# Kernel tuning notes

Measured on AMD Instinct MI355X. Metric: run time of the kernel, lower is better.

The kernel has to match this reference:

```python
import jax, jax.numpy as jnp
import numpy as np
import math

B, S, C = 4, 2048, 128
H, DK, DV, K = 8, 64, 64, 3


def setup_inputs() -> dict:
    key = jax.random.key(0)
    ks = jax.random.split(key, 12)
    sd = 0.05
    return {
        "x": jax.random.normal(ks[0], (B, S, C), dtype=jnp.float32),
        "length": jax.random.randint(ks[1], (B,), 1, S + 1, dtype=jnp.int32),
        "wq": jax.random.normal(ks[2], (H * DK, C, K), dtype=jnp.float32) * sd,
        "bq": jnp.zeros((H * DK,), dtype=jnp.float32),
        "wk": jax.random.normal(ks[3], (H * DK, C, K), dtype=jnp.float32) * sd,
        "bk": jnp.zeros((H * DK,), dtype=jnp.float32),
        "wv": jax.random.normal(ks[4], (H * DV, C), dtype=jnp.float32) * sd,
        "bv": jnp.zeros((H * DV,), dtype=jnp.float32),
        "w1": jax.random.normal(ks[5], (DV, H * DV), dtype=jnp.float32) * sd,
        "b1": jnp.zeros((DV,), dtype=jnp.float32),
        "w2": jax.random.normal(ks[6], (1, DV), dtype=jnp.float32) * sd,
        "b2": jnp.zeros((1,), dtype=jnp.float32),
    }


def _causal_conv(x, w, b):
    # x: (b,s,c), w: (o,c,k) torch Conv1d layout -> (b,s,o), causal (left) padding
    y = jax.lax.conv_general_dilated(
        x.transpose(0, 2, 1), w, window_strides=(1,), padding=[(K - 1, 0)],
        dimension_numbers=("NCH", "OIH", "NCH"))
    return y.transpose(0, 2, 1) + b


def _split_heads(x, d):
    b, s, _ = x.shape
    return x.reshape(b, s, H, d).transpose(0, 2, 1, 3)  # (b,h,s,d)


def reference(x, length, wq, bq, wk, bk, wv, bv, w1, b1, w2, b2):
    q = _split_heads(_causal_conv(x, wq, bq), DK)            # (b,h,s,dk)
    k = _split_heads(_causal_conv(x, wk, bk), DK)            # (b,h,s,dk)
    v = _split_heads(jax.nn.relu(x @ wv.T + bv), DV)         # (b,h,s,dv)

    attn = jnp.einsum("bhqd,bhkd->bhqk", q, k) / math.sqrt(DK)
    # future mask: additive -1e9 above the diagonal (matches triu * -1e9 + softmax)
    future = jnp.triu(jnp.ones((S, S), dtype=attn.dtype), k=1) * (-1e9)
    score = jax.nn.softmax(attn + future, axis=-1)
    # padding mask: zero query rows >= length[b]
    row_valid = (jnp.arange(S)[None, :] < length[:, None]).astype(score.dtype)
    score = score * row_valid[:, None, :, None]              # (b,h,s,s)

    out1 = jnp.einsum("bhqk,bhkd->bhqd", score, v)           # (b,h,s,dv)
    out2 = out1.transpose(0, 2, 1, 3).reshape(x.shape[0], S, H * DV)
    out3 = jax.nn.relu(out2 @ w1.T + b1) @ w2.T + b2         # (b,s,1)
    return out3, score
```

## Files before the change

### kernel.cpp

```cpp
#include <hip/hip_runtime.h>

#define S_ 2048
#define C_ 128
#define B_ 4
#define H_ 8
#define D_ 64

typedef __attribute__((ext_vector_type(8))) short bf16x8;
typedef __attribute__((ext_vector_type(4))) float f32x4;

__device__ inline unsigned short f2bf(float f) {
    union { float f; unsigned int u; } c; c.f = f;
    unsigned int u = c.u;
    unsigned int r = (u + 0x7FFFu + ((u >> 16) & 1u)) >> 16;
    return (unsigned short)r;
}
__device__ inline float bf2f(unsigned short s) {
    union { unsigned int u; float f; } c; c.u = ((unsigned int)s) << 16;
    return c.f;
}

__global__ __launch_bounds__(256) void prep_kernel(
    const float* __restrict__ x,
    const float* __restrict__ wq, const float* __restrict__ wk,
    const float* __restrict__ wv, const float* __restrict__ w1,
    unsigned short* __restrict__ xh,
    unsigned short* __restrict__ wPackQ, unsigned short* __restrict__ wPackK,
    unsigned short* __restrict__ wPackV, float* __restrict__ w1T)
{
    int idx = blockIdx.x * 256 + threadIdx.x;
    if (idx < 1048576) {
        xh[idx] = f2bf(x[idx]);
    } else if (idx < 1245184) {
        int i = idx - 1048576;
        int t = i >> 16, r = i & 65535;
        int o = r >> 7, c = r & 127;
        wPackQ[i] = f2bf(wq[o * 384 + c * 3 + t]);
    } else if (idx < 1441792) {
        int i = idx - 1245184;
        int t = i >> 16, r = i & 65535;
        int o = r >> 7, c = r & 127;
        wPackK[i] = f2bf(wk[o * 384 + c * 3 + t]);
    } else if (idx < 1507328) {
        int i = idx - 1441792;
        wPackV[i] = f2bf(wv[i]);
    } else if (idx < 1540096) {
        int i = idx - 1507328;
        int j = i >> 6, d = i & 63;
        w1T[i] = w1[d * 512 + j];
    }
}

__global__ __launch_bounds__(256) void qkv_kernel(
    const unsigned short* __restrict__ xh,
    const unsigned short* __restrict__ wPackQ, const unsigned short* __restrict__ wPackK,
    const unsigned short* __restrict__ wPackV,
    const float* __restrict__ bq, const float* __restrict__ bk,
    const float* __restrict__ bv,
    unsigned short* __restrict__ Qh, unsigned short* __restrict__ Kh,
    unsigned short* __restrict__ VhT)
{
    __shared__ __align__(16) short xs[130 * 136];
    __shared__ __align__(16) short ws[64 * 136];

    int s0 = blockIdx.x * 128;
    int h = blockIdx.y;
    int b = blockIdx.z;
    int bh = b * H_ + h;
    int tid = threadIdx.x;
    int w = tid >> 6;
    int lane = tid & 63;
    int col = lane & 15;
    int quad = lane >> 4;

    for (int i = tid; i < 2080; i += 256) {
        int row = i >> 4, c8 = (i & 15) << 3;
        int s = s0 - 2 + row;
        uint4 v = {0u, 0u, 0u, 0u};
        if (s >= 0) v = *(const uint4*)&xh[((long)b * S_ + s) * C_ + c8];
        *(uint4*)&xs[row * 136 + c8] = v;
    }

    for (int sec = 0; sec < 3; sec++) {
        const unsigned short* wsel = (sec == 0) ? wPackQ : (sec == 1) ? wPackK : wPackV;
        int tlo = (sec == 2) ? 2 : 0;

        f32x4 acc[2][4];
        #pragma unroll
        for (int rt = 0; rt < 2; rt++)
            #pragma unroll
            for (int nt = 0; nt < 4; nt++) acc[rt][nt] = (f32x4){0.f, 0.f, 0.f, 0.f};

        for (int t = tlo; t < 3; t++) {
            if (!(sec == 0 && t == 0)) __syncthreads();
            long wbase = (sec == 2) ? ((long)h * 8192)
                                    : ((long)t * 65536 + (long)h * 8192);
            for (int i = tid; i < 1024; i += 256) {
                int row = i >> 4, c8 = (i & 15) << 3;
                *(uint4*)&ws[row * 136 + c8] = *(const uint4*)&wsel[wbase + row * 128 + c8];
            }
            __syncthreads();

            #pragma unroll
            for (int kc = 0; kc < 4; kc++) {
                int ko = kc * 32 + quad * 8;
                bf16x8 a0 = *(const bf16x8*)&xs[(w * 32 + col + t) * 136 + ko];
                bf16x8 a1 = *(const bf16x8*)&xs[(w * 32 + 16 + col + t) * 136 + ko];
                #pragma unroll
                for (int nt = 0; nt < 4; nt++) {
                    bf16x8 bfr = *(const bf16x8*)&ws[(nt * 16 + col) * 136 + ko];
                    acc[0][nt] = __builtin_amdgcn_mfma_f32_16x16x32_bf16(a0, bfr, acc[0][nt], 0, 0, 0);
                    acc[1][nt] = __builtin_amdgcn_mfma_f32_16x16x32_bf16(a1, bfr, acc[1][nt], 0, 0, 0);
                }
            }
        }

        if (sec == 0) {
            #pragma unroll
            for (int nt = 0; nt < 4; nt++) {
                float bias = bq[h * 64 + nt * 16 + col];
                #pragma unroll
                for (int rt = 0; rt < 2; rt++)
                    #pragma unroll
                    for (int r = 0; r < 4; r++) {
                        int s = s0 + w * 32 + rt * 16 + quad * 4 + r;
                        Qh[((long)bh * S_ + s) * D_ + nt * 16 + col] =
                            f2bf((acc[rt][nt][r] + bias) * 0.125f);
                    }
            }
        } else if (sec == 1) {
            #pragma unroll
            for (int nt = 0; nt < 4; nt++) {
                float bias = bk[h * 64 + nt * 16 + col];
                #pragma unroll
                for (int rt = 0; rt < 2; rt++)
                    #pragma unroll
                    for (int r = 0; r < 4; r++) {
                        int s = s0 + w * 32 + rt * 16 + quad * 4 + r;
                        Kh[((long)bh * S_ + s) * D_ + nt * 16 + col] =
                            f2bf(acc[rt][nt][r] + bias);
                    }
            }
        } else {
            __syncthreads();
            #pragma unroll
            for (int nt = 0; nt < 4; nt++) {
                float bias = bv[h * 64 + nt * 16 + col];
                #pragma unroll
                for (int rt = 0; rt < 2; rt++)
                    #pragma unroll
                    for (int r = 0; r < 4; r++) {
                        int sl = w * 32 + rt * 16 + quad * 4 + r;
                        ws[(nt * 16 + col) * 136 + sl] =
                            (short)f2bf(fmaxf(acc[rt][nt][r] + bias, 0.f));
                    }
            }
            __syncthreads();
            for (int i = tid; i < 1024; i += 256) {
                int row = i >> 4, c8 = (i & 15) << 3;
                *(uint4*)&VhT[((long)bh * D_ + row) * S_ + s0 + c8] =
                    *(const uint4*)&ws[row * 136 + c8];
            }
        }
    }
}

#define PST 78
__global__ __launch_bounds__(256) void attn_kernel(
    const unsigned short* __restrict__ Qh, const unsigned short* __restrict__ Kh,
    const unsigned short* __restrict__ VhT, const int* __restrict__ length,
    float* __restrict__ score, float* __restrict__ out2)
{
    __shared__ __align__(16) short Kbuf[2][64 * 72];
    __shared__ __align__(16) short Pfh[64 * PST];

    int idx = blockIdx.x;
    int xcd = idx & 7;
    int slot = idx >> 3;
    int t = slot >> 2;
    int qt = (t < 16) ? t : 47 - t;
    int bh = xcd * 4 + (slot & 3);
    int b = bh >> 3, h = bh & 7;
    int q0 = qt * 64;
    int tid = threadIdx.x;
    int w = tid >> 6;
    int lane = tid & 63;
    int col = lane & 15;
    int quad = lane >> 4;
    int len = length[b];

    const unsigned short* Qb = Qh + (long)bh * S_ * D_;
    const unsigned short* Kb = Kh + (long)bh * S_ * D_;
    const unsigned short* Vtb = VhT + (long)bh * D_ * S_;
    float* scb = score + (long)bh * S_ * S_;

    int srow_ = tid >> 2, sc16_ = (tid & 3) * 16;

    {
        *(uint4*)&Pfh[srow_ * PST + sc16_]     = *(const uint4*)&Qb[(q0 + srow_) * D_ + sc16_];
        *(uint4*)&Pfh[srow_ * PST + sc16_ + 8] = *(const uint4*)&Qb[(q0 + srow_) * D_ + sc16_ + 8];
    }
    __syncthreads();
    int arow = w * 16 + col;
    bf16x8 aq0 = *(const bf16x8*)&Pfh[arow * PST + quad * 8];
    bf16x8 aq1 = *(const bf16x8*)&Pfh[arow * PST + 32 + quad * 8];

    float lrun[4];
    #pragma unroll
    for (int r = 0; r < 4; r++) lrun[r] = 0.f;

    {
        *(uint4*)&Kbuf[0][srow_ * 72 + sc16_]     = *(const uint4*)&Kb[srow_ * D_ + sc16_];
        *(uint4*)&Kbuf[0][srow_ * 72 + sc16_ + 8] = *(const uint4*)&Kb[srow_ * D_ + sc16_ + 8];
    }
    __syncthreads();

    for (int kt = 0; kt <= qt; kt++) {
        int buf = kt & 1;
        if (kt < qt) {
            *(uint4*)&Kbuf[1 - buf][srow_ * 72 + sc16_] =
                *(const uint4*)&Kb[((kt + 1) * 64 + srow_) * D_ + sc16_];
            *(uint4*)&Kbuf[1 - buf][srow_ * 72 + sc16_ + 8] =
                *(const uint4*)&Kb[((kt + 1) * 64 + srow_) * D_ + sc16_ + 8];
        }

        f32x4 acc[4];
        #pragma unroll
        for (int n = 0; n < 4; n++) acc[n] = (f32x4){0.f, 0.f, 0.f, 0.f};
        #pragma unroll
        for (int n = 0; n < 4; n++) {
            bf16x8 b0 = *(const bf16x8*)&Kbuf[buf][(n * 16 + col) * 72 + quad * 8];
            acc[n] = __builtin_amdgcn_mfma_f32_16x16x32_bf16(aq0, b0, acc[n], 0, 0, 0);
            bf16x8 b1 = *(const bf16x8*)&Kbuf[buf][(n * 16 + col) * 72 + 32 + quad * 8];
            acc[n] = __builtin_amdgcn_mfma_f32_16x16x32_bf16(aq1, b1, acc[n], 0, 0, 0);
        }
        if (kt == qt) {
            #pragma unroll
            for (int n = 0; n < 4; n++) {
                int kk = kt * 64 + n * 16 + col;
                #pragma unroll
                for (int r = 0; r < 4; r++) {
                    int q = q0 + w * 16 + quad * 4 + r;
                    if (kk > q) acc[n][r] = -1.0e30f;
                }
            }
        }
        #pragma unroll
        for (int r = 0; r < 4; r++) {
            lrun[r] += __expf(acc[0][r]) + __expf(acc[1][r]) +
                       __expf(acc[2][r]) + __expf(acc[3][r]);
        }
        __syncthreads();
    }

    #pragma unroll
    for (int off = 1; off < 16; off <<= 1) {
        #pragma unroll
        for (int r = 0; r < 4; r++) lrun[r] += __shfl_xor(lrun[r], off, 64);
    }
    float linv[4];
    #pragma unroll
    for (int r = 0; r < 4; r++) linv[r] = 1.0f / lrun[r];

    f32x4 oacc[4];
    #pragma unroll
    for (int n = 0; n < 4; n++) oacc[n] = (f32x4){0.f, 0.f, 0.f, 0.f};

    for (int kt = 0; kt <= qt; kt++) {
        __syncthreads();
        {
            *(uint4*)&Kbuf[0][srow_ * 72 + sc16_] =
                *(const uint4*)&Kb[(kt * 64 + srow_) * D_ + sc16_];
            *(uint4*)&Kbuf[0][srow_ * 72 + sc16_ + 8] =
                *(const uint4*)&Kb[(kt * 64 + srow_) * D_ + sc16_ + 8];
            *(uint4*)&Kbuf[1][srow_ * 72 + sc16_] =
                *(const uint4*)&Vtb[srow_ * S_ + kt * 64 + sc16_];
            *(uint4*)&Kbuf[1][srow_ * 72 + sc16_ + 8] =
                *(const uint4*)&Vtb[srow_ * S_ + kt * 64 + sc16_ + 8];
        }
        __syncthreads();

        f32x4 acc[4];
        #pragma unroll
        for (int n = 0; n < 4; n++) acc[n] = (f32x4){0.f, 0.f, 0.f, 0.f};
        #pragma unroll
        for (int n = 0; n < 4; n++) {
            bf16x8 b0 = *(const bf16x8*)&Kbuf[0][(n * 16 + col) * 72 + quad * 8];
            acc[n] = __builtin_amdgcn_mfma_f32_16x16x32_bf16(aq0, b0, acc[n], 0, 0, 0);
            bf16x8 b1 = *(const bf16x8*)&Kbuf[0][(n * 16 + col) * 72 + 32 + quad * 8];
            acc[n] = __builtin_amdgcn_mfma_f32_16x16x32_bf16(aq1, b1, acc[n], 0, 0, 0);
        }

        bool diag = (kt == qt);
        #pragma unroll
        for (int n = 0; n < 4; n++) {
            int kk = kt * 64 + n * 16 + col;
            #pragma unroll
            for (int r = 0; r < 4; r++) {
                int q = q0 + w * 16 + quad * 4 + r;
                float p = __expf(acc[n][r]) * linv[r];
                if (q >= len || (diag && kk > q)) p = 0.f;
                Pfh[(w * 16 + quad * 4 + r) * PST + n * 16 + col] = (short)f2bf(p);
            }
        }
        bf16x8 pa0 = *(const bf16x8*)&Pfh[(w * 16 + col) * PST + quad * 8];
        bf16x8 pa1 = *(const bf16x8*)&Pfh[(w * 16 + col) * PST + 32 + quad * 8];
        #pragma unroll
        for (int n = 0; n < 4; n++) {
            bf16x8 v0 = *(const bf16x8*)&Kbuf[1][(n * 16 + col) * 72 + quad * 8];
            oacc[n] = __builtin_amdgcn_mfma_f32_16x16x32_bf16(pa0, v0, oacc[n], 0, 0, 0);
            bf16x8 v1 = *(const bf16x8*)&Kbuf[1][(n * 16 + col) * 72 + 32 + quad * 8];
            oacc[n] = __builtin_amdgcn_mfma_f32_16x16x32_bf16(pa1, v1, oacc[n], 0, 0, 0);
        }

        {
            int rlo = lane >> 4;
            int c4 = (lane & 15) * 4;
            #pragma unroll
            for (int j = 0; j < 4; j++) {
                int row = w * 16 + j * 4 + rlo;
                uint2 pk = *(const uint2*)&Pfh[row * PST + c4];
                f32x4 v;
                v[0] = bf2f((unsigned short)(pk.x & 0xFFFFu));
                v[1] = bf2f((unsigned short)(pk.x >> 16));
                v[2] = bf2f((unsigned short)(pk.y & 0xFFFFu));
                v[3] = bf2f((unsigned short)(pk.y >> 16));
                __builtin_nontemporal_store(v,
                    (f32x4*)&scb[(long)(q0 + row) * S_ + kt * 64 + c4]);
            }
        }
    }

    #pragma unroll
    for (int n = 0; n < 4; n++) {
        #pragma unroll
        for (int r = 0; r < 4; r++) {
            int q = q0 + w * 16 + quad * 4 + r;
            out2[((long)(b * S_ + q)) * 512 + h * 64 + n * 16 + col] = oacc[n][r];
        }
    }

    f32x4 z = (f32x4){0.f, 0.f, 0.f, 0.f};
    for (int kt2 = qt + 1; kt2 < 32; kt2++) {
        #pragma unroll
        for (int it = 0; it < 4; it++) {
            int idx2 = tid + it * 256;
            int rr = idx2 >> 4, cc = idx2 & 15;
            __builtin_nontemporal_store(z,
                (f32x4*)&scb[(long)(q0 + rr) * S_ + kt2 * 64 + cc * 4]);
        }
    }
}

__global__ __launch_bounds__(256) void mlp_kernel(
    const float* __restrict__ out2, const float* __restrict__ w1T,
    const float* __restrict__ b1, const float* __restrict__ w2,
    const float* __restrict__ b2, float* __restrict__ out3)
{
    __shared__ float xr[2048];
    int sg0 = blockIdx.x * 4;
    int tid = threadIdx.x;
    for (int i = tid; i < 2048; i += 256) xr[i] = out2[(long)sg0 * 512 + i];
    __syncthreads();

    int sl = tid >> 6, d = tid & 63;
    float acc = 0.f;
    const float* xp = &xr[sl * 512];
    #pragma unroll 8
    for (int j = 0; j < 512; j++) acc += xp[j] * w1T[j * 64 + d];
    float hval = fmaxf(acc + b1[d], 0.f);
    float p = hval * w2[d];
    #pragma unroll
    for (int off = 32; off > 0; off >>= 1) p += __shfl_xor(p, off, 64);
    if (d == 0) out3[sg0 + sl] = p + b2[0];
}

extern "C" void kernel_launch(void* const* d_in, const int* in_sizes, int n_in,
                              void* d_out, int out_size, void* d_ws, size_t ws_size,
                              hipStream_t stream) {
    const float* x      = (const float*)d_in[0];
    const int*   length = (const int*)  d_in[1];
    const float* wq     = (const float*)d_in[2];
    const float* bq     = (const float*)d_in[3];
    const float* wk     = (const float*)d_in[4];
    const float* bk     = (const float*)d_in[5];
    const float* wv     = (const float*)d_in[6];
    const float* bv     = (const float*)d_in[7];
    const float* w1     = (const float*)d_in[8];
    const float* b1     = (const float*)d_in[9];
    const float* w2     = (const float*)d_in[10];
    const float* b2     = (const float*)d_in[11];

    float* out3  = (float*)d_out;
    float* score = (float*)d_out + 8192;

    float* ws  = (float*)d_ws;
    unsigned short* xh     = (unsigned short*)ws;  ws += 524288;
    unsigned short* wPackQ = (unsigned short*)ws;  ws += 98304;
    unsigned short* wPackK = (unsigned short*)ws;  ws += 98304;
    unsigned short* wPackV = (unsigned short*)ws;  ws += 32768;
    float* w1T = ws;  ws += 32768;
    unsigned short* Qh  = (unsigned short*)ws;  ws += 2097152;
    unsigned short* Kh  = (unsigned short*)ws;  ws += 2097152;
    unsigned short* VhT = (unsigned short*)ws;  ws += 2097152;
    float* o2  = ws;  ws += 4194304;

    hipLaunchKernelGGL(prep_kernel, dim3(6016), dim3(256), 0, stream,
                       x, wq, wk, wv, w1, xh, wPackQ, wPackK, wPackV, w1T);
    hipLaunchKernelGGL(qkv_kernel, dim3(16, 8, 4), dim3(256), 0, stream,
                       xh, wPackQ, wPackK, wPackV, bq, bk, bv, Qh, Kh, VhT);
    hipLaunchKernelGGL(attn_kernel, dim3(1024), dim3(256), 0, stream,
                       Qh, Kh, VhT, length, score, o2);
    hipLaunchKernelGGL(mlp_kernel, dim3(2048), dim3(256), 0, stream,
                       o2, w1T, b1, w2, b2, out3);
}
```

Baseline: 657.7 us.

## Load Q/K/V MFMA fragments straight from global, drop LDS staging and barriers

Q, K and V MFMA operand fragments are now read directly from global memory into registers instead of being staged through shared-memory tiles, which removes most __syncthreads barriers and the K/V LDS buffers. The 1/sqrt(d) scale is folded together with log2(e) into Q so softmax can use exp2f. Score values are now written as fp32 straight from registers with scalar nontemporal stores rather than re-read from LDS as bf16 and stored as 16-byte vectors. The P fragment is packed with v_cvt_pk_bf16_f32. The risks are more redundant global/L2 traffic, since several waves load the same K/V rows, and less coalesced score writes.

```diff
diff --git a/kernel.cpp b/kernel.cpp
--- a/kernel.cpp
+++ b/kernel.cpp
@@ -125,7 +125,7 @@
                     for (int r = 0; r < 4; r++) {
                         int s = s0 + w * 32 + rt * 16 + quad * 4 + r;
                         Qh[((long)bh * S_ + s) * D_ + nt * 16 + col] =
-                            f2bf((acc[rt][nt][r] + bias) * 0.125f);
+                            f2bf((acc[rt][nt][r] + bias) * 0.18033688011112042f);
                     }
             }
         } else if (sec == 1) {
@@ -171,7 +171,6 @@
     const unsigned short* __restrict__ VhT, const int* __restrict__ length,
     float* __restrict__ score, float* __restrict__ out2)
 {
-    __shared__ __align__(16) short Kbuf[2][64 * 72];
     __shared__ __align__(16) short Pfh[64 * PST];
 
     int idx = blockIdx.x;
@@ -194,45 +193,29 @@
     const unsigned short* Vtb = VhT + (long)bh * D_ * S_;
     float* scb = score + (long)bh * S_ * S_;
 
-    int srow_ = tid >> 2, sc16_ = (tid & 3) * 16;
-
-    {
-        *(uint4*)&Pfh[srow_ * PST + sc16_]     = *(const uint4*)&Qb[(q0 + srow_) * D_ + sc16_];
-        *(uint4*)&Pfh[srow_ * PST + sc16_ + 8] = *(const uint4*)&Qb[(q0 + srow_) * D_ + sc16_ + 8];
-    }
-    __syncthreads();
     int arow = w * 16 + col;
-    bf16x8 aq0 = *(const bf16x8*)&Pfh[arow * PST + quad * 8];
-    bf16x8 aq1 = *(const bf16x8*)&Pfh[arow * PST + 32 + quad * 8];
+    bf16x8 aq0 = *(const bf16x8*)&Qb[(q0 + arow) * D_ + quad * 8];
+    bf16x8 aq1 = *(const bf16x8*)&Qb[(q0 + arow) * D_ + 32 + quad * 8];
 
     float lrun[4];
     #pragma unroll
     for (int r = 0; r < 4; r++) lrun[r] = 0.f;
 
-    {
-        *(uint4*)&Kbuf[0][srow_ * 72 + sc16_]     = *(const uint4*)&Kb[srow_ * D_ + sc16_];
-        *(uint4*)&Kbuf[0][srow_ * 72 + sc16_ + 8] = *(const uint4*)&Kb[srow_ * D_ + sc16_ + 8];
-    }
-    __syncthreads();
-
     for (int kt = 0; kt <= qt; kt++) {
-        int buf = kt & 1;
-        if (kt < qt) {
-            *(uint4*)&Kbuf[1 - buf][srow_ * 72 + sc16_] =
-                *(const uint4*)&Kb[((kt + 1) * 64 + srow_) * D_ + sc16_];
-            *(uint4*)&Kbuf[1 - buf][srow_ * 72 + sc16_ + 8] =
-                *(const uint4*)&Kb[((kt + 1) * 64 + srow_) * D_ + sc16_ + 8];
-        }
-
+        bf16x8 kf0[4], kf1[4];
+        #pragma unroll
+        for (int n = 0; n < 4; n++) {
+            const unsigned short* kp = &Kb[(kt * 64 + n * 16 + col) * D_ + quad * 8];
+            kf0[n] = *(const bf16x8*)kp;
+            kf1[n] = *(const bf16x8*)(kp + 32);
+        }
         f32x4 acc[4];
         #pragma unroll
         for (int n = 0; n < 4; n++) acc[n] = (f32x4){0.f, 0.f, 0.f, 0.f};
         #pragma unroll
         for (int n = 0; n < 4; n++) {
-            bf16x8 b0 = *(const bf16x8*)&Kbuf[buf][(n * 16 + col) * 72 + quad * 8];
-            acc[n] = __builtin_amdgcn_mfma_f32_16x16x32_bf16(aq0, b0, acc[n], 0, 0, 0);
-            bf16x8 b1 = *(const bf16x8*)&Kbuf[buf][(n * 16 + col) * 72 + 32 + quad * 8];
-            acc[n] = __builtin_amdgcn_mfma_f32_16x16x32_bf16(aq1, b1, acc[n], 0, 0, 0);
+            acc[n] = __builtin_amdgcn_mfma_f32_16x16x32_bf16(aq0, kf0[n], acc[n], 0, 0, 0);
+            acc[n] = __builtin_amdgcn_mfma_f32_16x16x32_bf16(aq1, kf1[n], acc[n], 0, 0, 0);
         }
         if (kt == qt) {
             #pragma unroll
@@ -247,10 +230,9 @@
         }
         #pragma unroll
         for (int r = 0; r < 4; r++) {
-            lrun[r] += __expf(acc[0][r]) + __expf(acc[1][r]) +
-                       __expf(acc[2][r]) + __expf(acc[3][r]);
-        }
-        __syncthreads();
+            lrun[r] += exp2f(acc[0][r]) + exp2f(acc[1][r]) +
+                       exp2f(acc[2][r]) + exp2f(acc[3][r]);
+        }
     }
 
     #pragma unroll
@@ -266,68 +248,60 @@
     #pragma unroll
     for (int n = 0; n < 4; n++) oacc[n] = (f32x4){0.f, 0.f, 0.f, 0.f};
 
+    int prow = w * 16 + quad * 4;
     for (int kt = 0; kt <= qt; kt++) {
-        __syncthreads();
-        {
-            *(uint4*)&Kbuf[0][srow_ * 72 + sc16_] =
-                *(const uint4*)&Kb[(kt * 64 + srow_) * D_ + sc16_];
-            *(uint4*)&Kbuf[0][srow_ * 72 + sc16_ + 8] =
-                *(const uint4*)&Kb[(kt * 64 + srow_) * D_ + sc16_ + 8];
-            *(uint4*)&Kbuf[1][srow_ * 72 + sc16_] =
-                *(const uint4*)&Vtb[srow_ * S_ + kt * 64 + sc16_];
-            *(uint4*)&Kbuf[1][srow_ * 72 + sc16_ + 8] =
-                *(const uint4*)&Vtb[srow_ * S_ + kt * 64 + sc16_ + 8];
-        }
-        __syncthreads();
+        bf16x8 kf0[4], kf1[4], vf0[4], vf1[4];
+        #pragma unroll
+        for (int n = 0; n < 4; n++) {
+            const unsigned short* kp = &Kb[(kt * 64 + n * 16 + col) * D_ + quad * 8];
+            kf0[n] = *(const bf16x8*)kp;
+            kf1[n] = *(const bf16x8*)(kp + 32);
+        }
+        #pragma unroll
+        for (int n = 0; n < 4; n++) {
+            const unsigned short* vp = &Vtb[(n * 16 + col) * S_ + kt * 64 + quad * 8];
+            vf0[n] = *(const bf16x8*)vp;
+            vf1[n] = *(const bf16x8*)(vp + 32);
+        }
 
         f32x4 acc[4];
         #pragma unroll
         for (int n = 0; n < 4; n++) acc[n] = (f32x4){0.f, 0.f, 0.f, 0.f};
         #pragma unroll
         for (int n = 0; n < 4; n++) {
-            bf16x8 b0 = *(const bf16x8*)&Kbuf[0][(n * 16 + col) * 72 + quad * 8];
-            acc[n] = __builtin_amdgcn_mfma_f32_16x16x32_bf16(aq0, b0, acc[n], 0, 0, 0);
-            bf16x8 b1 = *(const bf16x8*)&Kbuf[0][(n * 16 + col) * 72 + 32 + quad * 8];
-            acc[n] = __builtin_amdgcn_mfma_f32_16x16x32_bf16(aq1, b1, acc[n], 0, 0, 0);
+            acc[n] = __builtin_amdgcn_mfma_f32_16x16x32_bf16(aq0, kf0[n], acc[n], 0, 0, 0);
+            acc[n] = __builtin_amdgcn_mfma_f32_16x16x32_bf16(aq1, kf1[n], acc[n], 0, 0, 0);
         }
 
         bool diag = (kt == qt);
         #pragma unroll
         for (int n = 0; n < 4; n++) {
             int kk = kt * 64 + n * 16 + col;
+            float p[4];
             #pragma unroll
             for (int r = 0; r < 4; r++) {
-                int q = q0 + w * 16 + quad * 4 + r;
-                float p = __expf(acc[n][r]) * linv[r];
-                if (q >= len || (diag && kk > q)) p = 0.f;
-                Pfh[(w * 16 + quad * 4 + r) * PST + n * 16 + col] = (short)f2bf(p);
-            }
-        }
+                int q = q0 + prow + r;
+                float pv = exp2f(acc[n][r]) * linv[r];
+                if (q >= len || (diag && kk > q)) pv = 0.f;
+                p[r] = pv;
+                __builtin_nontemporal_store(pv, &scb[(long)q * S_ + kk]);
+            }
+            unsigned int pk01, pk23;
+            asm("v_cvt_pk_bf16_f32 %0, %1, %2" : "=v"(pk01) : "v"(p[0]), "v"(p[1]));
+            asm("v_cvt_pk_bf16_f32 %0, %1, %2" : "=v"(pk23) : "v"(p[2]), "v"(p[3]));
+            int pcol = n * 16 + col;
+            Pfh[prow * PST + pcol]       = (short)(pk01 & 0xFFFFu);
+            Pfh[(prow + 1) * PST + pcol] = (short)(pk01 >> 16);
+            Pfh[(prow + 2) * PST + pcol] = (short)(pk23 & 0xFFFFu);
+            Pfh[(prow + 3) * PST + pcol] = (short)(pk23 >> 16);
+        }
+
         bf16x8 pa0 = *(const bf16x8*)&Pfh[(w * 16 + col) * PST + quad * 8];
         bf16x8 pa1 = *(const bf16x8*)&Pfh[(w * 16 + col) * PST + 32 + quad * 8];
         #pragma unroll
         for (int n = 0; n < 4; n++) {
-            bf16x8 v0 = *(const bf16x8*)&Kbuf[1][(n * 16 + col) * 72 + quad * 8];
-            oacc[n] = __builtin_amdgcn_mfma_f32_16x16x32_bf16(pa0, v0, oacc[n], 0, 0, 0);
-            bf16x8 v1 = *(const bf16x8*)&Kbuf[1][(n * 16 + col) * 72 + 32 + quad * 8];
-            oacc[n] = __builtin_amdgcn_mfma_f32_16x16x32_bf16(pa1, v1, oacc[n], 0, 0, 0);
-        }
-
-        {
-            int rlo = lane >> 4;
-            int c4 = (lane & 15) * 4;
-            #pragma unroll
-            for (int j = 0; j < 4; j++) {
-                int row = w * 16 + j * 4 + rlo;
-                uint2 pk = *(const uint2*)&Pfh[row * PST + c4];
-                f32x4 v;
-                v[0] = bf2f((unsigned short)(pk.x & 0xFFFFu));
-                v[1] = bf2f((unsigned short)(pk.x >> 16));
-                v[2] = bf2f((unsigned short)(pk.y & 0xFFFFu));
-                v[3] = bf2f((unsigned short)(pk.y >> 16));
-                __builtin_nontemporal_store(v,
-                    (f32x4*)&scb[(long)(q0 + row) * S_ + kt * 64 + c4]);
-            }
+            oacc[n] = __builtin_amdgcn_mfma_f32_16x16x32_bf16(pa0, vf0[n], oacc[n], 0, 0, 0);
+            oacc[n] = __builtin_amdgcn_mfma_f32_16x16x32_bf16(pa1, vf1[n], oacc[n], 0, 0, 0);
         }
     }
 
```

Result: slower. 759.1 us (+15.4%).
